# Optimization experiments

Measured on AMD Instinct MI355X. Metric: run time of the kernel, lower is better.

The kernel has to match this reference:

```python
import jax, jax.numpy as jnp
import numpy as np

D_MODEL = 1024
N_EXPERTS = 8
TOP_K = 2
D_FF = 4 * D_MODEL
BATCH, SEQ = 4, 2048


def setup_inputs() -> dict:
    key = jax.random.key(0)
    ks = jax.random.split(key, 7)
    s = 0.02
    return {
        "x": jax.random.normal(ks[0], (BATCH, SEQ, D_MODEL), dtype=jnp.float32),
        "Wg": jax.random.normal(ks[1], (D_MODEL, N_EXPERTS), dtype=jnp.float32) * s,
        "bg": jnp.zeros((N_EXPERTS,), dtype=jnp.float32),
        "W1": jax.random.normal(ks[2], (N_EXPERTS, D_MODEL, D_FF), dtype=jnp.float32) * s,
        "b1": jnp.zeros((N_EXPERTS, D_FF), dtype=jnp.float32),
        "W2": jax.random.normal(ks[3], (N_EXPERTS, D_FF, D_MODEL), dtype=jnp.float32) * s,
        "b2": jnp.zeros((N_EXPERTS, D_MODEL), dtype=jnp.float32),
    }


def reference(x, Wg, bg, W1, b1, W2, b2):
    B, S, D = x.shape
    T = B * S
    xf = x.reshape(T, D)  # [T, d_model]

    # Gating: top-k over softmax probabilities
    gate_logits = xf @ Wg + bg                      # [T, E]
    probs = jax.nn.softmax(gate_logits, axis=-1)
    weights, indices = jax.lax.top_k(probs, TOP_K)  # [T, K] each

    # Dense combine weights c[t, e] = sum_k weights[t,k] * (indices[t,k]==e)
    E = Wg.shape[1]
    c = jnp.zeros((T, E), dtype=x.dtype).at[jnp.arange(T)[:, None], indices].add(weights)

    # All-expert FFN as batched GEMMs (same math as masked per-expert loop)
    h = jnp.einsum('td,edf->etf', xf, W1) + b1[:, None, :]   # [E, T, d_ff]
    a = jax.nn.gelu(h, approximate=False)
    y = jnp.einsum('etf,efd->etd', a, W2) + b2[:, None, :]   # [E, T, d_model]

    out = jnp.einsum('te,etd->td', c, y).reshape(B, S, D)
    return out, gate_logits
```

## Files before the change

kernel.cpp:

```cpp
#include <hip/hip_runtime.h>
#include <hip/hip_bf16.h>
#include <math.h>

#define D_MODEL 1024
#define N_EXP   8
#define D_FF    4096
#define T_TOK   8192
#define NPAIR   (T_TOK * 2)
#define CAP_ROWS (NPAIR + N_EXP * 128)
#define MAX_T256 72
#define BKB 128

typedef __attribute__((ext_vector_type(4)))  float  f32x4;
typedef __attribute__((ext_vector_type(16))) float  f32x16;
typedef __attribute__((ext_vector_type(8)))  __bf16 bf16x8;
typedef __attribute__((ext_vector_type(4)))  __bf16 bf16x4;

#define OFF_W1T   0
#define OFF_W2T   67108864
#define OFF_H     134217728
#define OFF_XR    276824064
#define OFF_META  312475648
#define M_PAIREXP 0
#define M_PAIRW   65536
#define M_ROW2P   131072
#define M_COUNTS  200704
#define M_PADST   200736
#define M_CURSOR  200768
#define M_T2E     201792
#define M_TROW    202336
#define M_TLIM    202880

__device__ __forceinline__ void async_copy16(const void* g, void* s) {
  __builtin_amdgcn_global_load_lds(
      (const __attribute__((address_space(1))) void*)g,
      (__attribute__((address_space(3))) void*)s, 16, 0, 0);
}

__device__ __forceinline__ void wg_barrier() {
  asm volatile("" ::: "memory");
  __builtin_amdgcn_s_barrier();
  asm volatile("" ::: "memory");
}

__device__ __forceinline__ float gelu_fast(float v) {
  float u = 1.5957691216057308f * (v + 0.044715f * v * v * v);
  return v * __builtin_amdgcn_rcpf(1.f + __expf(-u));
}

__global__ void k_gate(const float* __restrict__ x, const float* __restrict__ Wg,
                       const float* __restrict__ bg, float* __restrict__ logits_out,
                       int* __restrict__ pairExpert, float* __restrict__ pairW) {
  const int t    = blockIdx.x * 4 + (threadIdx.x >> 6);
  const int lane = threadIdx.x & 63;
  const float* xp = x + (size_t)t * D_MODEL;
  float acc[8];
#pragma unroll
  for (int e = 0; e < 8; e++) acc[e] = 0.f;
#pragma unroll
  for (int i = 0; i < 16; i++) {
    int d = i * 64 + lane;
    float xv = xp[d];
    const float4* wr = (const float4*)(Wg + d * 8);
    float4 w0 = wr[0], w1 = wr[1];
    acc[0] += xv * w0.x; acc[1] += xv * w0.y; acc[2] += xv * w0.z; acc[3] += xv * w0.w;
    acc[4] += xv * w1.x; acc[5] += xv * w1.y; acc[6] += xv * w1.z; acc[7] += xv * w1.w;
  }
#pragma unroll
  for (int e = 0; e < 8; e++)
#pragma unroll
    for (int off = 32; off > 0; off >>= 1) acc[e] += __shfl_down(acc[e], off);
  if (lane == 0) {
    float l[8];
#pragma unroll
    for (int e = 0; e < 8; e++) { l[e] = acc[e] + bg[e]; logits_out[t * 8 + e] = l[e]; }
    float m = l[0];
#pragma unroll
    for (int e = 1; e < 8; e++) m = fmaxf(m, l[e]);
    float p[8], s = 0.f;
#pragma unroll
    for (int e = 0; e < 8; e++) { p[e] = expf(l[e] - m); s += p[e]; }
    float inv = 1.0f / s;
    int i1 = 0;
#pragma unroll
    for (int e = 1; e < 8; e++) if (l[e] > l[i1]) i1 = e;
    int i2 = (i1 == 0) ? 1 : 0;
#pragma unroll
    for (int e = 0; e < 8; e++) if (e != i1 && l[e] > l[i2]) i2 = e;
    pairExpert[t * 2 + 0] = i1; pairW[t * 2 + 0] = p[i1] * inv;
    pairExpert[t * 2 + 1] = i2; pairW[t * 2 + 1] = p[i2] * inv;
  }
}

__global__ void k_init(int* __restrict__ row2pair) {
  int i = blockIdx.x * 256 + threadIdx.x;
  if (i < CAP_ROWS) row2pair[i] = -1;
}

__global__ void k_offsets(const int* __restrict__ pairExpert, int* __restrict__ counts,
                          int* __restrict__ padStart, int* __restrict__ cursor,
                          int* __restrict__ t2e, int* __restrict__ trow,
                          int* __restrict__ tlim) {
  __shared__ int hist[8];
  int tid = threadIdx.x;
  if (tid < 8) hist[tid] = 0;
  __syncthreads();
  for (int i = tid; i < NPAIR; i += 256) atomicAdd(&hist[pairExpert[i]], 1);
  __syncthreads();
  if (tid == 0) {
    int run = 0, nt = 0;
    for (int e = 0; e < 8; e++) {
      counts[e] = hist[e]; padStart[e] = run; cursor[e * 32] = 0;
      int rows = ((hist[e] + 127) >> 7) << 7;
      for (int r0 = 0; r0 < rows; r0 += 256) {
        t2e[nt] = e; trow[nt] = run + r0;
        int rem = rows - r0;
        tlim[nt] = rem < 256 ? rem : 256;
        nt++;
      }
      run += rows;
    }
    for (; nt < MAX_T256; nt++) t2e[nt] = -1;
  }
}

__global__ void k_place(const int* __restrict__ pairExpert, const int* __restrict__ padStart,
                        int* __restrict__ cursor, int* __restrict__ row2pair) {
  int p = blockIdx.x * 256 + threadIdx.x;
  if (p >= NPAIR) return;
  int e = pairExpert[p];
  int r = atomicAdd(&cursor[e * 32], 1);
  row2pair[padStart[e] + r] = p;
}

__global__ void k_gather(const float* __restrict__ x, const int* __restrict__ row2pair,
                         __bf16* __restrict__ XR) {
  int row = blockIdx.x;
  int pair = row2pair[row];
  int c = threadIdx.x * 4;
  __bf16* dst = XR + (size_t)row * D_MODEL + c;
  if (pair < 0) {
    bf16x4 z = {(__bf16)0.f, (__bf16)0.f, (__bf16)0.f, (__bf16)0.f};
    *(bf16x4*)dst = z;
  } else {
    int t = pair >> 1;
    float4 v = *(const float4*)(x + (size_t)t * D_MODEL + c);
    bf16x4 o = {(__bf16)v.x, (__bf16)v.y, (__bf16)v.z, (__bf16)v.w};
    *(bf16x4*)dst = o;
  }
}

__global__ void k_convT(const float* __restrict__ in, __bf16* __restrict__ out,
                        int R, int C) {
  __shared__ __bf16 tile[64][68];
  int e = blockIdx.z;
  const float* ip = in + (size_t)e * R * C + (size_t)(blockIdx.y * 64) * C + blockIdx.x * 64;
  __bf16* op = out + (size_t)e * R * C + (size_t)(blockIdx.x * 64) * R + blockIdx.y * 64;
#pragma unroll
  for (int it = 0; it < 4; it++) {
    int idx = it * 1024 + threadIdx.x * 4;
    int lr = idx >> 6, lc = idx & 63;
    float4 v = *(const float4*)(ip + (size_t)lr * C + lc);
    bf16x4 o = {(__bf16)v.x, (__bf16)v.y, (__bf16)v.z, (__bf16)v.w};
    *(bf16x4*)&tile[lr][lc] = o;
  }
  __syncthreads();
#pragma unroll
  for (int it = 0; it < 4; it++) {
    int idx = it * 1024 + threadIdx.x * 4;
    int lc = idx >> 6, lr = idx & 63;
    bf16x4 o = {tile[lr + 0][lc], tile[lr + 1][lc], tile[lr + 2][lc], tile[lr + 3][lc]};
    *(bf16x4*)(op + (size_t)lc * R + lr) = o;
  }
}


__global__ __launch_bounds__(512, 2) void k_gemm1(
    const __bf16* __restrict__ XR, const __bf16* __restrict__ W1T,
    const float* __restrict__ b1, __bf16* __restrict__ H,
    const int* __restrict__ t2e, const int* __restrict__ trow,
    const int* __restrict__ tlim) {
  __shared__ __align__(16) char lds[2][65536];
  const int mt = blockIdx.y;
  const int e = t2e[mt];
  if (e < 0) return;
  const int rowBase = trow[mt];
  const int lim = tlim[mt];
  const int n0 = blockIdx.x * 256;

  const int tid = threadIdx.x;
  const int l = tid & 63;
  const int w = tid >> 6;
  const int wm = (w >> 2) * 128;
  const int wn = (w & 3) * 64;
  const int l31 = l & 31;
  const int rsub = l >> 3;
  const int sg = (l & 7) ^ rsub;

  const char* srcA[4]; const char* srcB[4];
#pragma unroll
  for (int i = 0; i < 4; i++) {
    int ra = rowBase + 8 * (w + 8 * i) + rsub;
    if (ra > CAP_ROWS - 1) ra = CAP_ROWS - 1;
    srcA[i] = (const char*)(XR + (size_t)ra * D_MODEL) + sg * 16;
    int rb = n0 + 8 * (w + 8 * i) + rsub;
    srcB[i] = (const char*)(W1T + (size_t)e * ((size_t)D_FF * D_MODEL)
                                + (size_t)rb * D_MODEL) + sg * 16;
  }
  const int axr = ((l >> 5) ^ (l & 7)) << 4;

  f32x16 acc[4][2];
#pragma unroll
  for (int i = 0; i < 4; i++)
#pragma unroll
    for (int j = 0; j < 2; j++) acc[i][j] = (f32x16)(0.f);

  {
    char* sAw = &lds[0][0];
    char* sBw = sAw + 32768;
#pragma unroll
    for (int i = 0; i < 4; i++) {
      async_copy16(srcA[i], sAw + (w + 8 * i) * 1024);
      async_copy16(srcB[i], sBw + (w + 8 * i) * 1024);
    }
    asm volatile("s_waitcnt vmcnt(0)" ::: "memory");
    wg_barrier();
  }

  bf16x8 A[2][4], B[2][4];
#pragma unroll 2
  for (int t = 0; t < 16; t++) {
    const int slot = t & 1;
    const char* sAr = &lds[0][0] + slot * 65536;
    const char* sBr = sAr + 32768;
    char* sAw = &lds[0][0] + (slot ^ 1) * 65536;
    char* sBw = sAw + 32768;
    const bool hn = (t + 1) < 16;
    const size_t ko = (size_t)(t + 1) * BKB;

    if (hn) {
      async_copy16(srcA[0] + ko, sAw + w * 1024);
      async_copy16(srcB[0] + ko, sBw + w * 1024);
      asm volatile("s_waitcnt vmcnt(2)" ::: "memory");
    } else {
      asm volatile("s_waitcnt vmcnt(0)" ::: "memory");
    }
    wg_barrier();
#pragma unroll
    for (int f = 0; f < 2; f++)
#pragma unroll
      for (int kc = 0; kc < 4; kc++)
        A[f][kc] = *(const bf16x8*)(sAr + (wm + f * 32 + l31) * BKB + (axr ^ (kc << 5)));
#pragma unroll
    for (int kc = 0; kc < 4; kc++)
      B[0][kc] = *(const bf16x8*)(sBr + (wn + l31) * BKB + (axr ^ (kc << 5)));
    __builtin_amdgcn_s_setprio(1);
#pragma unroll
    for (int kc = 0; kc < 4; kc++)
#pragma unroll
      for (int f = 0; f < 2; f++)
        acc[f][0] = __builtin_amdgcn_mfma_f32_32x32x16_bf16(A[f][kc], B[0][kc], acc[f][0], 0, 0, 0);
    __builtin_amdgcn_s_setprio(0);
    wg_barrier();

#pragma unroll
    for (int kc = 0; kc < 4; kc++)
      B[1][kc] = *(const bf16x8*)(sBr + (wn + 32 + l31) * BKB + (axr ^ (kc << 5)));
    if (hn) {
      async_copy16(srcA[1] + ko, sAw + (8 + w) * 1024);
      async_copy16(srcB[1] + ko, sBw + (8 + w) * 1024);
    }
    wg_barrier();
    __builtin_amdgcn_s_setprio(1);
#pragma unroll
    for (int kc = 0; kc < 4; kc++)
#pragma unroll
      for (int f = 0; f < 2; f++)
        acc[f][1] = __builtin_amdgcn_mfma_f32_32x32x16_bf16(A[f][kc], B[1][kc], acc[f][1], 0, 0, 0);
    __builtin_amdgcn_s_setprio(0);
    wg_barrier();

#pragma unroll
    for (int f = 0; f < 2; f++)
#pragma unroll
      for (int kc = 0; kc < 4; kc++)
        A[f][kc] = *(const bf16x8*)(sAr + (wm + 64 + f * 32 + l31) * BKB + (axr ^ (kc << 5)));
    if (hn) {
      async_copy16(srcA[2] + ko, sAw + (16 + w) * 1024);
      async_copy16(srcB[2] + ko, sBw + (16 + w) * 1024);
    }
    wg_barrier();
    __builtin_amdgcn_s_setprio(1);
#pragma unroll
    for (int kc = 0; kc < 4; kc++)
#pragma unroll
      for (int f = 0; f < 2; f++)
        acc[2 + f][0] = __builtin_amdgcn_mfma_f32_32x32x16_bf16(A[f][kc], B[0][kc], acc[2 + f][0], 0, 0, 0);
    __builtin_amdgcn_s_setprio(0);
    wg_barrier();

    if (hn) {
      async_copy16(srcA[3] + ko, sAw + (24 + w) * 1024);
      async_copy16(srcB[3] + ko, sBw + (24 + w) * 1024);
    }
    wg_barrier();
    __builtin_amdgcn_s_setprio(1);
#pragma unroll
    for (int kc = 0; kc < 4; kc++)
#pragma unroll
      for (int f = 0; f < 2; f++)
        acc[2 + f][1] = __builtin_amdgcn_mfma_f32_32x32x16_bf16(A[f][kc], B[1][kc], acc[2 + f][1], 0, 0, 0);
    __builtin_amdgcn_s_setprio(0);
    wg_barrier();
  }

  const int half = l >> 5;
  int colv[2]; float biasv[2];
#pragma unroll
  for (int tj = 0; tj < 2; tj++) {
    colv[tj] = n0 + wn + tj * 32 + l31;
    biasv[tj] = b1[e * D_FF + colv[tj]];
  }
#pragma unroll
  for (int ti = 0; ti < 4; ti++)
#pragma unroll
    for (int r = 0; r < 16; r++) {
      int lr = wm + ti * 32 + (r & 3) + 8 * (r >> 2) + 4 * half;
      if (lr < lim) {
        size_t row = (size_t)(rowBase + lr);
#pragma unroll
        for (int tj = 0; tj < 2; tj++)
          H[row * D_FF + colv[tj]] = (__bf16)gelu_fast(acc[ti][tj][r] + biasv[tj]);
      }
    }
}

__global__ __launch_bounds__(512, 2) void k_gemm2(
    const __bf16* __restrict__ H, const __bf16* __restrict__ W2T,
    const float* __restrict__ b2, float* __restrict__ out,
    const int* __restrict__ row2pair, const float* __restrict__ pairW,
    const int* __restrict__ t2e, const int* __restrict__ trow,
    const int* __restrict__ tlim) {
  __shared__ __align__(16) char lds[2][49152];
  const int mt = blockIdx.y;
  const int e = t2e[mt];
  if (e < 0) return;
  const int rowBase = trow[mt];
  const int lim = tlim[mt];
  const int n0 = blockIdx.x * 128;

  const int tid = threadIdx.x;
  const int l = tid & 63;
  const int w = tid >> 6;
  const int wm = (w >> 1) * 64;
  const int wn = (w & 1) * 64;
  const int l31 = l & 31;
  const int rsub = l >> 3;
  const int sg = (l & 7) ^ rsub;

  const char* srcA[4]; const char* srcB[2];
#pragma unroll
  for (int i = 0; i < 4; i++) {
    int ra = rowBase + 8 * (w + 8 * i) + rsub;
    if (ra > CAP_ROWS - 1) ra = CAP_ROWS - 1;
    srcA[i] = (const char*)(H + (size_t)ra * D_FF) + sg * 16;
  }
#pragma unroll
  for (int i = 0; i < 2; i++) {
    int rb = n0 + 8 * (w + 8 * i) + rsub;
    srcB[i] = (const char*)(W2T + (size_t)e * ((size_t)D_MODEL * D_FF)
                                + (size_t)rb * D_FF) + sg * 16;
  }
  const int axr = ((l >> 5) ^ (l & 7)) << 4;

  f32x16 acc[2][2];
#pragma unroll
  for (int i = 0; i < 2; i++)
#pragma unroll
    for (int j = 0; j < 2; j++) acc[i][j] = (f32x16)(0.f);

  {
    char* sAw = &lds[0][0];
    char* sBw = sAw + 32768;
#pragma unroll
    for (int i = 0; i < 4; i++) async_copy16(srcA[i], sAw + (w + 8 * i) * 1024);
#pragma unroll
    for (int i = 0; i < 2; i++) async_copy16(srcB[i], sBw + (w + 8 * i) * 1024);
    asm volatile("s_waitcnt vmcnt(0)" ::: "memory");
    wg_barrier();
  }

  bf16x8 A[4], B[2][4];
#pragma unroll 2
  for (int t = 0; t < 64; t++) {
    const int slot = t & 1;
    const char* sAr = &lds[0][0] + slot * 49152;
    const char* sBr = sAr + 32768;
    char* sAw = &lds[0][0] + (slot ^ 1) * 49152;
    char* sBw = sAw + 32768;
    const bool hn = (t + 1) < 64;
    const size_t ko = (size_t)(t + 1) * BKB;

    if (hn) {
      async_copy16(srcA[0] + ko, sAw + w * 1024);
      async_copy16(srcB[0] + ko, sBw + w * 1024);
      async_copy16(srcA[1] + ko, sAw + (8 + w) * 1024);
      async_copy16(srcB[1] + ko, sBw + (8 + w) * 1024);
      asm volatile("s_waitcnt vmcnt(4)" ::: "memory");
    } else {
      asm volatile("s_waitcnt vmcnt(0)" ::: "memory");
    }
    wg_barrier();
#pragma unroll
    for (int kc = 0; kc < 4; kc++)
      A[kc] = *(const bf16x8*)(sAr + (wm + l31) * BKB + (axr ^ (kc << 5)));
#pragma unroll
    for (int tj = 0; tj < 2; tj++)
#pragma unroll
      for (int kc = 0; kc < 4; kc++)
        B[tj][kc] = *(const bf16x8*)(sBr + (wn + tj * 32 + l31) * BKB + (axr ^ (kc << 5)));
    __builtin_amdgcn_s_setprio(1);
#pragma unroll
    for (int kc = 0; kc < 4; kc++)
#pragma unroll
      for (int tj = 0; tj < 2; tj++)
        acc[0][tj] = __builtin_amdgcn_mfma_f32_32x32x16_bf16(A[kc], B[tj][kc], acc[0][tj], 0, 0, 0);
    __builtin_amdgcn_s_setprio(0);
    wg_barrier();

#pragma unroll
    for (int kc = 0; kc < 4; kc++)
      A[kc] = *(const bf16x8*)(sAr + (wm + 32 + l31) * BKB + (axr ^ (kc << 5)));
    if (hn) {
      async_copy16(srcA[2] + ko, sAw + (16 + w) * 1024);
      async_copy16(srcA[3] + ko, sAw + (24 + w) * 1024);
    }
    wg_barrier();
    __builtin_amdgcn_s_setprio(1);
#pragma unroll
    for (int kc = 0; kc < 4; kc++)
#pragma unroll
      for (int tj = 0; tj < 2; tj++)
        acc[1][tj] = __builtin_amdgcn_mfma_f32_32x32x16_bf16(A[kc], B[tj][kc], acc[1][tj], 0, 0, 0);
    __builtin_amdgcn_s_setprio(0);
    wg_barrier();
  }

  const int half = l >> 5;
  int colv[2]; float biasv[2];
#pragma unroll
  for (int tj = 0; tj < 2; tj++) {
    colv[tj] = n0 + wn + tj * 32 + l31;
    biasv[tj] = b2[e * D_MODEL + colv[tj]];
  }
#pragma unroll
  for (int ti = 0; ti < 2; ti++)
#pragma unroll
    for (int r = 0; r < 16; r++) {
      int lr = wm + ti * 32 + (r & 3) + 8 * (r >> 2) + 4 * half;
      if (lr >= lim) continue;
      int pair = row2pair[rowBase + lr];
      if (pair < 0) continue;
      float pw = pairW[pair];
      size_t tok = (size_t)(pair >> 1);
#pragma unroll
      for (int tj = 0; tj < 2; tj++)
        atomicAdd(out + tok * D_MODEL + colv[tj], pw * (acc[ti][tj][r] + biasv[tj]));
    }
}

extern "C" void kernel_launch(void* const* d_in, const int* in_sizes, int n_in,
                              void* d_out, int out_size, void* d_ws, size_t ws_size,
                              hipStream_t stream) {
  const float* x  = (const float*)d_in[0];
  const float* Wg = (const float*)d_in[1];
  const float* bg = (const float*)d_in[2];
  const float* W1 = (const float*)d_in[3];
  const float* b1 = (const float*)d_in[4];
  const float* W2 = (const float*)d_in[5];
  const float* b2 = (const float*)d_in[6];
  float* out        = (float*)d_out;
  float* logits_out = out + (size_t)T_TOK * D_MODEL;

  char* ws = (char*)d_ws;
  __bf16* W1T = (__bf16*)(ws + OFF_W1T);
  __bf16* W2T = (__bf16*)(ws + OFF_W2T);
  __bf16* H   = (__bf16*)(ws + OFF_H);
  __bf16* XR  = (__bf16*)(ws + OFF_XR);
  char* meta = ws + OFF_META;
  int*   pairExpert = (int*)(meta + M_PAIREXP);
  float* pairW      = (float*)(meta + M_PAIRW);
  int*   row2pair   = (int*)(meta + M_ROW2P);
  int*   counts     = (int*)(meta + M_COUNTS);
  int*   padStart   = (int*)(meta + M_PADST);
  int*   cursor     = (int*)(meta + M_CURSOR);
  int*   t2e        = (int*)(meta + M_T2E);
  int*   trow       = (int*)(meta + M_TROW);
  int*   tlim       = (int*)(meta + M_TLIM);

  hipMemsetAsync(out, 0, (size_t)T_TOK * D_MODEL * sizeof(float), stream);

  k_convT<<<dim3(D_FF / 64, D_MODEL / 64, N_EXP), 256, 0, stream>>>(W1, W1T, D_MODEL, D_FF);
  k_convT<<<dim3(D_MODEL / 64, D_FF / 64, N_EXP), 256, 0, stream>>>(W2, W2T, D_FF, D_MODEL);

  k_init<<<(CAP_ROWS + 255) / 256, 256, 0, stream>>>(row2pair);
  k_gate<<<T_TOK / 4, 256, 0, stream>>>(x, Wg, bg, logits_out, pairExpert, pairW);
  k_offsets<<<1, 256, 0, stream>>>(pairExpert, counts, padStart, cursor, t2e, trow, tlim);
  k_place<<<NPAIR / 256, 256, 0, stream>>>(pairExpert, padStart, cursor, row2pair);
  k_gather<<<CAP_ROWS, 256, 0, stream>>>(x, row2pair, XR);

  k_gemm1<<<dim3(D_FF / 256, MAX_T256), 512, 0, stream>>>(XR, W1T, b1, H, t2e, trow, tlim);
  k_gemm2<<<dim3(D_MODEL / 128, MAX_T256), 512, 0, stream>>>(H, W2T, b2, out, row2pair, pairW,
                                                             t2e, trow, tlim);
}
```

Measured before the change: 952.5 us.

## Use triple-buffered LDS pipeline and 256x128 tiles for both expert GEMMs

Both grouped GEMMs now use a three-slot LDS ring. The global-to-LDS copy for tile t+2 is issued while tile t is being computed, and there is a single barrier per K step instead of several barriers inside each step. GEMM1's tile shrinks from 256x256 to 256x128 so the two kernels share one loop body, which doubles GEMM1's grid and its reloads of the A operand. The 144KB of LDS per block may limit residency to one block per CU, undercutting the launch_bounds hint of two.

```diff
diff --git a/kernel.cpp b/kernel.cpp
--- a/kernel.cpp
+++ b/kernel.cpp
@@ -10,6 +10,7 @@
 #define CAP_ROWS (NPAIR + N_EXP * 128)
 #define MAX_T256 72
 #define BKB 128
+#define SLOT 49152
 
 typedef __attribute__((ext_vector_type(4)))  float  f32x4;
 typedef __attribute__((ext_vector_type(16))) float  f32x16;
@@ -175,162 +176,128 @@
 }
 
 
+#define STAGE(SW, T)                                                       \
+  do {                                                                     \
+    size_t _ko = (size_t)(T) * BKB;                                        \
+    _Pragma("unroll")                                                      \
+    for (int _i = 0; _i < 4; _i++)                                         \
+      async_copy16(srcA[_i] + _ko, (SW) + (w + 8 * _i) * 1024);            \
+    _Pragma("unroll")                                                      \
+    for (int _i = 0; _i < 2; _i++)                                         \
+      async_copy16(srcB[_i] + _ko, (SW) + 32768 + (w + 8 * _i) * 1024);    \
+  } while (0)
+
+#define LOADFRAG(SR)                                                       \
+  _Pragma("unroll")                                                        \
+  for (int _mi = 0; _mi < 2; _mi++)                                        \
+    _Pragma("unroll")                                                      \
+    for (int _kc = 0; _kc < 4; _kc++)                                      \
+      Af[_mi][_kc] = *(const bf16x8*)((SR) + (wm + _mi * 32 + l31) * BKB + (axr ^ (_kc << 5))); \
+  _Pragma("unroll")                                                        \
+  for (int _nj = 0; _nj < 2; _nj++)                                        \
+    _Pragma("unroll")                                                      \
+    for (int _kc = 0; _kc < 4; _kc++)                                      \
+      Bf[_nj][_kc] = *(const bf16x8*)((SR) + 32768 + (wn + _nj * 32 + l31) * BKB + (axr ^ (_kc << 5)));
+
+#define MFMAS                                                              \
+  __builtin_amdgcn_s_setprio(1);                                           \
+  _Pragma("unroll")                                                        \
+  for (int _kc = 0; _kc < 4; _kc++)                                        \
+    _Pragma("unroll")                                                      \
+    for (int _mi = 0; _mi < 2; _mi++)                                      \
+      _Pragma("unroll")                                                    \
+      for (int _nj = 0; _nj < 2; _nj++)                                    \
+        acc[_mi][_nj] = __builtin_amdgcn_mfma_f32_32x32x16_bf16(           \
+            Af[_mi][_kc], Bf[_nj][_kc], acc[_mi][_nj], 0, 0, 0);           \
+  __builtin_amdgcn_s_setprio(0);
+
+#define BODY_MAIN(T, SR, SW)                                               \
+  do { bf16x8 Af[2][4], Bf[2][4]; LOADFRAG(SR); STAGE(SW, (T) + 2); MFMAS; \
+       asm volatile("s_waitcnt vmcnt(6)" ::: "memory"); wg_barrier(); } while (0)
+#define BODY_NOST(SR)                                                      \
+  do { bf16x8 Af[2][4], Bf[2][4]; LOADFRAG(SR); MFMAS;                     \
+       asm volatile("s_waitcnt vmcnt(0)" ::: "memory"); wg_barrier(); } while (0)
+#define BODY_LAST(SR)                                                      \
+  do { bf16x8 Af[2][4], Bf[2][4]; LOADFRAG(SR); MFMAS; } while (0)
+
 __global__ __launch_bounds__(512, 2) void k_gemm1(
     const __bf16* __restrict__ XR, const __bf16* __restrict__ W1T,
     const float* __restrict__ b1, __bf16* __restrict__ H,
     const int* __restrict__ t2e, const int* __restrict__ trow,
     const int* __restrict__ tlim) {
-  __shared__ __align__(16) char lds[2][65536];
+  __shared__ __align__(16) char lds[3][SLOT];
   const int mt = blockIdx.y;
   const int e = t2e[mt];
   if (e < 0) return;
   const int rowBase = trow[mt];
   const int lim = tlim[mt];
-  const int n0 = blockIdx.x * 256;
+  const int n0 = blockIdx.x * 128;
 
   const int tid = threadIdx.x;
   const int l = tid & 63;
   const int w = tid >> 6;
-  const int wm = (w >> 2) * 128;
-  const int wn = (w & 3) * 64;
+  const int wm = (w >> 1) * 64;
+  const int wn = (w & 1) * 64;
   const int l31 = l & 31;
+  const int half = l >> 5;
   const int rsub = l >> 3;
   const int sg = (l & 7) ^ rsub;
 
-  const char* srcA[4]; const char* srcB[4];
+  const char* srcA[4]; const char* srcB[2];
 #pragma unroll
   for (int i = 0; i < 4; i++) {
     int ra = rowBase + 8 * (w + 8 * i) + rsub;
     if (ra > CAP_ROWS - 1) ra = CAP_ROWS - 1;
     srcA[i] = (const char*)(XR + (size_t)ra * D_MODEL) + sg * 16;
+  }
+#pragma unroll
+  for (int i = 0; i < 2; i++) {
     int rb = n0 + 8 * (w + 8 * i) + rsub;
     srcB[i] = (const char*)(W1T + (size_t)e * ((size_t)D_FF * D_MODEL)
                                 + (size_t)rb * D_MODEL) + sg * 16;
   }
   const int axr = ((l >> 5) ^ (l & 7)) << 4;
 
-  f32x16 acc[4][2];
-#pragma unroll
-  for (int i = 0; i < 4; i++)
+  f32x16 acc[2][2];
+#pragma unroll
+  for (int i = 0; i < 2; i++)
 #pragma unroll
     for (int j = 0; j < 2; j++) acc[i][j] = (f32x16)(0.f);
 
-  {
-    char* sAw = &lds[0][0];
-    char* sBw = sAw + 32768;
-#pragma unroll
-    for (int i = 0; i < 4; i++) {
-      async_copy16(srcA[i], sAw + (w + 8 * i) * 1024);
-      async_copy16(srcB[i], sBw + (w + 8 * i) * 1024);
-    }
-    asm volatile("s_waitcnt vmcnt(0)" ::: "memory");
-    wg_barrier();
-  }
-
-  bf16x8 A[2][4], B[2][4];
-#pragma unroll 2
-  for (int t = 0; t < 16; t++) {
-    const int slot = t & 1;
-    const char* sAr = &lds[0][0] + slot * 65536;
-    const char* sBr = sAr + 32768;
-    char* sAw = &lds[0][0] + (slot ^ 1) * 65536;
-    char* sBw = sAw + 32768;
-    const bool hn = (t + 1) < 16;
-    const size_t ko = (size_t)(t + 1) * BKB;
-
-    if (hn) {
-      async_copy16(srcA[0] + ko, sAw + w * 1024);
-      async_copy16(srcB[0] + ko, sBw + w * 1024);
-      asm volatile("s_waitcnt vmcnt(2)" ::: "memory");
-    } else {
-      asm volatile("s_waitcnt vmcnt(0)" ::: "memory");
-    }
-    wg_barrier();
-#pragma unroll
-    for (int f = 0; f < 2; f++)
-#pragma unroll
-      for (int kc = 0; kc < 4; kc++)
-        A[f][kc] = *(const bf16x8*)(sAr + (wm + f * 32 + l31) * BKB + (axr ^ (kc << 5)));
-#pragma unroll
-    for (int kc = 0; kc < 4; kc++)
-      B[0][kc] = *(const bf16x8*)(sBr + (wn + l31) * BKB + (axr ^ (kc << 5)));
-    __builtin_amdgcn_s_setprio(1);
-#pragma unroll
-    for (int kc = 0; kc < 4; kc++)
-#pragma unroll
-      for (int f = 0; f < 2; f++)
-        acc[f][0] = __builtin_amdgcn_mfma_f32_32x32x16_bf16(A[f][kc], B[0][kc], acc[f][0], 0, 0, 0);
-    __builtin_amdgcn_s_setprio(0);
-    wg_barrier();
-
-#pragma unroll
-    for (int kc = 0; kc < 4; kc++)
-      B[1][kc] = *(const bf16x8*)(sBr + (wn + 32 + l31) * BKB + (axr ^ (kc << 5)));
-    if (hn) {
-      async_copy16(srcA[1] + ko, sAw + (8 + w) * 1024);
-      async_copy16(srcB[1] + ko, sBw + (8 + w) * 1024);
-    }
-    wg_barrier();
-    __builtin_amdgcn_s_setprio(1);
-#pragma unroll
-    for (int kc = 0; kc < 4; kc++)
-#pragma unroll
-      for (int f = 0; f < 2; f++)
-        acc[f][1] = __builtin_amdgcn_mfma_f32_32x32x16_bf16(A[f][kc], B[1][kc], acc[f][1], 0, 0, 0);
-    __builtin_amdgcn_s_setprio(0);
-    wg_barrier();
-
-#pragma unroll
-    for (int f = 0; f < 2; f++)
-#pragma unroll
-      for (int kc = 0; kc < 4; kc++)
-        A[f][kc] = *(const bf16x8*)(sAr + (wm + 64 + f * 32 + l31) * BKB + (axr ^ (kc << 5)));
-    if (hn) {
-      async_copy16(srcA[2] + ko, sAw + (16 + w) * 1024);
-      async_copy16(srcB[2] + ko, sBw + (16 + w) * 1024);
-    }
-    wg_barrier();
-    __builtin_amdgcn_s_setprio(1);
-#pragma unroll
-    for (int kc = 0; kc < 4; kc++)
-#pragma unroll
-      for (int f = 0; f < 2; f++)
-        acc[2 + f][0] = __builtin_amdgcn_mfma_f32_32x32x16_bf16(A[f][kc], B[0][kc], acc[2 + f][0], 0, 0, 0);
-    __builtin_amdgcn_s_setprio(0);
-    wg_barrier();
-
-    if (hn) {
-      async_copy16(srcA[3] + ko, sAw + (24 + w) * 1024);
-      async_copy16(srcB[3] + ko, sBw + (24 + w) * 1024);
-    }
-    wg_barrier();
-    __builtin_amdgcn_s_setprio(1);
-#pragma unroll
-    for (int kc = 0; kc < 4; kc++)
-#pragma unroll
-      for (int f = 0; f < 2; f++)
-        acc[2 + f][1] = __builtin_amdgcn_mfma_f32_32x32x16_bf16(A[f][kc], B[1][kc], acc[2 + f][1], 0, 0, 0);
-    __builtin_amdgcn_s_setprio(0);
-    wg_barrier();
-  }
-
-  const int half = l >> 5;
+  char* s0 = &lds[0][0]; char* s1 = &lds[1][0]; char* s2 = &lds[2][0];
+
+  STAGE(s0, 0);
+  STAGE(s1, 1);
+  asm volatile("s_waitcnt vmcnt(6)" ::: "memory");
+  wg_barrier();
+
+#pragma unroll 1
+  for (int tg = 0; tg < 4; tg++) {
+    BODY_MAIN(3 * tg + 0, s0, s2);
+    BODY_MAIN(3 * tg + 1, s1, s0);
+    BODY_MAIN(3 * tg + 2, s2, s1);
+  }
+  BODY_MAIN(12, s0, s2);
+  BODY_MAIN(13, s1, s0);
+  BODY_NOST(s2);
+  BODY_LAST(s0);
+
   int colv[2]; float biasv[2];
 #pragma unroll
-  for (int tj = 0; tj < 2; tj++) {
-    colv[tj] = n0 + wn + tj * 32 + l31;
-    biasv[tj] = b1[e * D_FF + colv[tj]];
-  }
-#pragma unroll
-  for (int ti = 0; ti < 4; ti++)
+  for (int nj = 0; nj < 2; nj++) {
+    colv[nj] = n0 + wn + nj * 32 + l31;
+    biasv[nj] = b1[e * D_FF + colv[nj]];
+  }
+#pragma unroll
+  for (int mi = 0; mi < 2; mi++)
 #pragma unroll
     for (int r = 0; r < 16; r++) {
-      int lr = wm + ti * 32 + (r & 3) + 8 * (r >> 2) + 4 * half;
+      int lr = wm + mi * 32 + (r & 3) + 8 * (r >> 2) + 4 * half;
       if (lr < lim) {
         size_t row = (size_t)(rowBase + lr);
 #pragma unroll
-        for (int tj = 0; tj < 2; tj++)
-          H[row * D_FF + colv[tj]] = (__bf16)gelu_fast(acc[ti][tj][r] + biasv[tj]);
+        for (int nj = 0; nj < 2; nj++)
+          H[row * D_FF + colv[nj]] = (__bf16)gelu_fast(acc[mi][nj][r] + biasv[nj]);
       }
     }
 }
@@ -341,7 +308,7 @@
     const int* __restrict__ row2pair, const float* __restrict__ pairW,
     const int* __restrict__ t2e, const int* __restrict__ trow,
     const int* __restrict__ tlim) {
-  __shared__ __align__(16) char lds[2][49152];
+  __shared__ __align__(16) char lds[3][SLOT];
   const int mt = blockIdx.y;
   const int e = t2e[mt];
   if (e < 0) return;
@@ -355,6 +322,7 @@
   const int wm = (w >> 1) * 64;
   const int wn = (w & 1) * 64;
   const int l31 = l & 31;
+  const int half = l >> 5;
   const int rsub = l >> 3;
   const int sg = (l & 7) ^ rsub;
 
@@ -379,93 +347,43 @@
 #pragma unroll
     for (int j = 0; j < 2; j++) acc[i][j] = (f32x16)(0.f);
 
-  {
-    char* sAw = &lds[0][0];
-    char* sBw = sAw + 32768;
-#pragma unroll
-    for (int i = 0; i < 4; i++) async_copy16(srcA[i], sAw + (w + 8 * i) * 1024);
-#pragma unroll
-    for (int i = 0; i < 2; i++) async_copy16(srcB[i], sBw + (w + 8 * i) * 1024);
-    asm volatile("s_waitcnt vmcnt(0)" ::: "memory");
-    wg_barrier();
-  }
-
-  bf16x8 A[4], B[2][4];
-#pragma unroll 2
-  for (int t = 0; t < 64; t++) {
-    const int slot = t & 1;
-    const char* sAr = &lds[0][0] + slot * 49152;
-    const char* sBr = sAr + 32768;
-    char* sAw = &lds[0][0] + (slot ^ 1) * 49152;
-    char* sBw = sAw + 32768;
-    const bool hn = (t + 1) < 64;
-    const size_t ko = (size_t)(t + 1) * BKB;
-
-    if (hn) {
-      async_copy16(srcA[0] + ko, sAw + w * 1024);
-      async_copy16(srcB[0] + ko, sBw + w * 1024);
-      async_copy16(srcA[1] + ko, sAw + (8 + w) * 1024);
-      async_copy16(srcB[1] + ko, sBw + (8 + w) * 1024);
-      asm volatile("s_waitcnt vmcnt(4)" ::: "memory");
-    } else {
-      asm volatile("s_waitcnt vmcnt(0)" ::: "memory");
-    }
-    wg_barrier();
-#pragma unroll
-    for (int kc = 0; kc < 4; kc++)
-      A[kc] = *(const bf16x8*)(sAr + (wm + l31) * BKB + (axr ^ (kc << 5)));
-#pragma unroll
-    for (int tj = 0; tj < 2; tj++)
-#pragma unroll
-      for (int kc = 0; kc < 4; kc++)
-        B[tj][kc] = *(const bf16x8*)(sBr + (wn + tj * 32 + l31) * BKB + (axr ^ (kc << 5)));
-    __builtin_amdgcn_s_setprio(1);
-#pragma unroll
-    for (int kc = 0; kc < 4; kc++)
-#pragma unroll
-      for (int tj = 0; tj < 2; tj++)
-        acc[0][tj] = __builtin_amdgcn_mfma_f32_32x32x16_bf16(A[kc], B[tj][kc], acc[0][tj], 0, 0, 0);
-    __builtin_amdgcn_s_setprio(0);
-    wg_barrier();
-
-#pragma unroll
-    for (int kc = 0; kc < 4; kc++)
-      A[kc] = *(const bf16x8*)(sAr + (wm + 32 + l31) * BKB + (axr ^ (kc << 5)));
-    if (hn) {
-      async_copy16(srcA[2] + ko, sAw + (16 + w) * 1024);
-      async_copy16(srcA[3] + ko, sAw + (24 + w) * 1024);
-    }
-    wg_barrier();
-    __builtin_amdgcn_s_setprio(1);
-#pragma unroll
-    for (int kc = 0; kc < 4; kc++)
-#pragma unroll
-      for (int tj = 0; tj < 2; tj++)
-        acc[1][tj] = __builtin_amdgcn_mfma_f32_32x32x16_bf16(A[kc], B[tj][kc], acc[1][tj], 0, 0, 0);
-    __builtin_amdgcn_s_setprio(0);
-    wg_barrier();
-  }
-
-  const int half = l >> 5;
+  char* s0 = &lds[0][0]; char* s1 = &lds[1][0]; char* s2 = &lds[2][0];
+
+  STAGE(s0, 0);
+  STAGE(s1, 1);
+  asm volatile("s_waitcnt vmcnt(6)" ::: "memory");
+  wg_barrier();
+
+#pragma unroll 1
+  for (int tg = 0; tg < 20; tg++) {
+    BODY_MAIN(3 * tg + 0, s0, s2);
+    BODY_MAIN(3 * tg + 1, s1, s0);
+    BODY_MAIN(3 * tg + 2, s2, s1);
+  }
+  BODY_MAIN(60, s0, s2);
+  BODY_MAIN(61, s1, s0);
+  BODY_NOST(s2);
+  BODY_LAST(s0);
+
   int colv[2]; float biasv[2];
 #pragma unroll
-  for (int tj = 0; tj < 2; tj++) {
-    colv[tj] = n0 + wn + tj * 32 + l31;
-    biasv[tj] = b2[e * D_MODEL + colv[tj]];
-  }
-#pragma unroll
-  for (int ti = 0; ti < 2; ti++)
+  for (int nj = 0; nj < 2; nj++) {
+    colv[nj] = n0 + wn + nj * 32 + l31;
+    biasv[nj] = b2[e * D_MODEL + colv[nj]];
+  }
+#pragma unroll
+  for (int mi = 0; mi < 2; mi++)
 #pragma unroll
     for (int r = 0; r < 16; r++) {
-      int lr = wm + ti * 32 + (r & 3) + 8 * (r >> 2) + 4 * half;
+      int lr = wm + mi * 32 + (r & 3) + 8 * (r >> 2) + 4 * half;
       if (lr >= lim) continue;
       int pair = row2pair[rowBase + lr];
       if (pair < 0) continue;
       float pw = pairW[pair];
       size_t tok = (size_t)(pair >> 1);
 #pragma unroll
-      for (int tj = 0; tj < 2; tj++)
-        atomicAdd(out + tok * D_MODEL + colv[tj], pw * (acc[ti][tj][r] + biasv[tj]));
+      for (int nj = 0; nj < 2; nj++)
+        atomicAdd(out + tok * D_MODEL + colv[nj], pw * (acc[mi][nj][r] + biasv[nj]));
     }
 }
 
@@ -509,7 +427,7 @@
   k_place<<<NPAIR / 256, 256, 0, stream>>>(pairExpert, padStart, cursor, row2pair);
   k_gather<<<CAP_ROWS, 256, 0, stream>>>(x, row2pair, XR);
 
-  k_gemm1<<<dim3(D_FF / 256, MAX_T256), 512, 0, stream>>>(XR, W1T, b1, H, t2e, trow, tlim);
+  k_gemm1<<<dim3(D_FF / 128, MAX_T256), 512, 0, stream>>>(XR, W1T, b1, H, t2e, trow, tlim);
   k_gemm2<<<dim3(D_MODEL / 128, MAX_T256), 512, 0, stream>>>(H, W2T, b2, out, row2pair, pairW,
                                                              t2e, trow, tlim);
 }
```

New measurement: 932.5 us. 2.1% less time.
